# Optimization experiments

Measured on AMD Instinct MI355X. Metric: run time of the kernel, lower is better.

## Reference

```python
import jax, jax.numpy as jnp
import numpy as np

N, K, D, M, P, HG, HD = 120000, 8, 64, 100000, 16, 32, 96
VOXEL, TAU, OCC_INC, LMIN, LMAX = 0.1, 0.3, 0.5, -2.0, 3.5


def setup_inputs() -> dict:
    ks = jax.random.split(jax.random.key(0), 20)
    f32 = jnp.float32
    s = 0.05
    return {
        'pts_xyz': jax.random.uniform(ks[0], (N, 3), f32) * 10.0,
        'f_pts': jax.random.normal(ks[1], (N, D), f32),
        'z_latent': jax.random.normal(ks[2], (M, D), f32),
        'vals_st': jax.random.normal(ks[3], (M,), f32) * 0.5,
        'centers_xyz': jax.random.uniform(ks[4], (M, 3), f32) * 10.0,
        'Wf': jax.random.normal(ks[5], (P, D), f32) * s,
        'Wz': jax.random.normal(ks[6], (P, D), f32) * s,
        'w_delta': jax.random.normal(ks[7], (1, 3), f32) * s,
        'b_delta': jnp.zeros((1,), f32),
        'log_temp': jnp.zeros((1,), f32),
        'W_ih': jax.random.normal(ks[8], (3 * D, D), f32) * s,
        'W_hh': jax.random.normal(ks[9], (3 * D, D), f32) * s,
        'b_ih': jnp.zeros((3 * D,), f32),
        'b_hh': jnp.zeros((3 * D,), f32),
        'Wg1': jax.random.normal(ks[10], (HG, 2 * D), f32) * s,
        'bg1': jnp.zeros((HG,), f32),
        'Wg2': jax.random.normal(ks[11], (1, HG), f32) * s,
        'bg2': jnp.zeros((1,), f32),
        'ln_g': jnp.ones((D,), f32),
        'ln_b': jnp.zeros((D,), f32),
        'Wd1': jax.random.normal(ks[12], (HD, D), f32) * s,
        'bd1': jnp.zeros((HD,), f32),
        'Wd2': jax.random.normal(ks[13], (HD, HD), f32) * s,
        'bd2': jnp.zeros((HD,), f32),
        'Wd3': jax.random.normal(ks[14], (1, HD), f32) * s,
        'bd3': jnp.zeros((1,), f32),
        'keys': jnp.sort(jax.random.randint(ks[15], (M,), 0, 2 ** 30, jnp.int32)),
        'cand_idx': jax.random.randint(ks[16], (N, K), 0, M, jnp.int32),
    }


def _forward(pts_xyz, f_pts, z_latent, vals_st, centers_xyz, Wf, Wz, w_delta, b_delta,
             log_temp, W_ih, W_hh, b_ih, b_hh, Wg1, bg1, Wg2, bg2, ln_g, ln_b,
             Wd1, bd1, Wd2, bd2, Wd3, bd3, keys, cand_idx):
    # --- sparse voxel hash lookup + log-odds scatter update ---
    ijk = jnp.floor(pts_xyz / VOXEL).astype(jnp.int32)
    off = jnp.int32(1 << 9)
    h = ((ijk[:, 0] + off) << 20) ^ ((ijk[:, 1] + off) << 10) ^ (ijk[:, 2] + off)
    vox_idx = jnp.clip(jnp.searchsorted(keys, h), 0, M - 1)  # (N,)
    vals_new = jnp.clip(vals_st.at[vox_idx].add(OCC_INC), LMIN, LMAX)

    # --- top-K low-temperature routing: sim(f, z, delta) ---
    z_c = z_latent[cand_idx]                                  # (N,K,D) gather
    delta = pts_xyz[:, None, :] - centers_xyz[cand_idx]       # (N,K,3)
    Fp = f_pts @ Wf.T                                         # (N,P)
    Zp = z_c @ Wz.T                                           # (N,K,P)
    Fp = Fp / (jnp.linalg.norm(Fp, axis=-1, keepdims=True) + 1e-6)
    Zp = Zp / (jnp.linalg.norm(Zp, axis=-1, keepdims=True) + 1e-6)
    core = jnp.einsum('np,nkp->nk', Fp, Zp)
    dterm = jnp.einsum('nkc,c->nk', delta, w_delta[0]) + b_delta[0]
    sim = jnp.exp(log_temp[0]) * (core + dterm)
    w = jax.nn.softmax(sim / TAU, axis=-1)                    # (N,K)

    # --- scatter weighted point features to voxels ---
    flat_idx = cand_idx.reshape(-1)                           # (N*K,)
    contrib = (w[..., None] * f_pts[:, None, :]).reshape(-1, D)
    msg = jax.ops.segment_sum(contrib, flat_idx, num_segments=M)   # (M,D)
    wsum = jax.ops.segment_sum(w.reshape(-1), flat_idx, num_segments=M)
    msg = msg / (wsum[:, None] + 1e-6)

    # --- per-voxel gate + GRU latent fusion ---
    gate_in = jnp.concatenate([z_latent, msg], axis=-1)       # (M,2D)
    g = jax.nn.sigmoid(jax.nn.relu(gate_in @ Wg1.T + bg1) @ Wg2.T + bg2)  # (M,1)
    gi = msg @ W_ih.T + b_ih
    gh = z_latent @ W_hh.T + b_hh
    gir, giz, gin = jnp.split(gi, 3, axis=-1)
    ghr, ghz, ghn = jnp.split(gh, 3, axis=-1)
    r = jax.nn.sigmoid(gir + ghr)
    u = jax.nn.sigmoid(giz + ghz)
    n = jnp.tanh(gin + r * ghn)
    h_new = (1.0 - u) * n + u * z_latent
    z_new = z_latent + g * (h_new - z_latent)                 # (M,D)

    # --- decode occupancy: LN -> fc1 -> residual fc2 -> fc3 -> sigmoid ---
    mu = z_new.mean(-1, keepdims=True)
    var = z_new.var(-1, keepdims=True)
    x = (z_new - mu) * jax.lax.rsqrt(var + 1e-5) * ln_g + ln_b
    hd = jax.nn.relu(x @ Wd1.T + bd1)
    hd = hd + jax.nn.relu(hd @ Wd2.T + bd2)
    p = jax.nn.sigmoid((hd @ Wd3.T + bd3)[:, 0])              # (M,)

    return jnp.concatenate([p, vals_new])                     # (2M,)


def reference(pts_xyz, f_pts, z_latent, vals_st, centers_xyz, Wf, Wz, w_delta, b_delta,
              log_temp, W_ih, W_hh, b_ih, b_hh, Wg1, bg1, Wg2, bg2, ln_g, ln_b,
              Wd1, bd1, Wd2, bd2, Wd3, bd3, keys, cand_idx):
    return _forward(pts_xyz, f_pts, z_latent, vals_st, centers_xyz, Wf, Wz, w_delta,
                    b_delta, log_temp, W_ih, W_hh, b_ih, b_hh, Wg1, bg1, Wg2, bg2,
                    ln_g, ln_b, Wd1, bd1, Wd2, bd2, Wd3, bd3, keys, cand_idx)
```

## Files before the change

kernel.cpp:

```cpp
#include <hip/hip_runtime.h>
#include <math.h>

#define Nn 120000
#define Kk 8
#define Dd 64
#define Mm 100000
#define Pp 16
#define HGg 32
#define HDd 96
#define CAP 40
#define LUTB 12

typedef __attribute__((ext_vector_type(8))) short bf16x8;
typedef __attribute__((ext_vector_type(4))) float f32x4;
typedef __attribute__((ext_vector_type(4))) float fx4;
typedef __attribute__((ext_vector_type(4))) int ix4;

#define PB_K0    1563
#define PB_PREP  (PB_K0 + 3750)
#define PB_PACK  (PB_PREP + 22)
#define PB_INIT  (PB_PACK + 391)

__device__ __forceinline__ float sigmoidf_(float x) { return 1.f / (1.f + __expf(-x)); }
__device__ __forceinline__ float tanh_fast(float x) {
    float e = __expf(2.f * x);
    return 1.f - 2.f / (e + 1.f);
}
__device__ __forceinline__ short f2bf(float f) {
    unsigned u = __float_as_uint(f);
    unsigned r = (u + 0x7fffu + ((u >> 16) & 1u)) >> 16;
    return (short)r;
}

__global__ __launch_bounds__(256) void k_prep_all(const float* __restrict__ z,
                                                  const float* __restrict__ Wz,
                                                  const float* __restrict__ centers,
                                                  const float* __restrict__ w_delta,
                                                  const int* __restrict__ keys,
                                                  const float* __restrict__ f_pts,
                                                  const float* __restrict__ Wg1,
                                                  const float* __restrict__ W_ih,
                                                  const float* __restrict__ W_hh,
                                                  const float* __restrict__ Wd1,
                                                  const float* __restrict__ Wd2,
                                                  const float* __restrict__ vals,
                                                  unsigned* __restrict__ Zbf,
                                                  float* __restrict__ cdot,
                                                  int* __restrict__ lut,
                                                  signed char* __restrict__ f8,
                                                  short* __restrict__ wsW,
                                                  int* __restrict__ cnt,
                                                  float* __restrict__ vacc) {
    int b = blockIdx.x;
    if (b < PB_K0) {
        int g = threadIdx.x & 3;
        int m = b * 64 + (threadIdx.x >> 2);
        if (m >= Mm) return;
        if (g == 0 && m <= (1 << LUTB)) {
            int target = m << (30 - LUTB);
            int lo = 0, hi = Mm;
            while (lo < hi) {
                int mid = (lo + hi) >> 1;
                if (keys[mid] < target) lo = mid + 1; else hi = mid;
            }
            lut[m] = lo;
        }
        const float4* zr = (const float4*)(z + (size_t)m * Dd + g * 16);
        float4 q0 = zr[0], q1 = zr[1], q2 = zr[2], q3 = zr[3];
        float acc[Pp];
#pragma unroll
        for (int p = 0; p < Pp; p++) {
            const float4* w = (const float4*)(Wz + (size_t)p * Dd + g * 16);
            float4 w0 = w[0], w1 = w[1], w2 = w[2], w3 = w[3];
            float s = q0.x * w0.x + q0.y * w0.y + q0.z * w0.z + q0.w * w0.w;
            s += q1.x * w1.x + q1.y * w1.y + q1.z * w1.z + q1.w * w1.w;
            s += q2.x * w2.x + q2.y * w2.y + q2.z * w2.z + q2.w * w2.w;
            s += q3.x * w3.x + q3.y * w3.y + q3.z * w3.z + q3.w * w3.w;
            acc[p] = s;
        }
#pragma unroll
        for (int p = 0; p < Pp; p++) {
            acc[p] += __shfl_xor(acc[p], 1, 64);
            acc[p] += __shfl_xor(acc[p], 2, 64);
        }
        float ss = 0.f;
#pragma unroll
        for (int p = 0; p < Pp; p++) ss = fmaf(acc[p], acc[p], ss);
        float inv = 1.f / (sqrtf(ss) + 1e-6f);
        unsigned* row = Zbf + (size_t)m * 8;
        if (g < 2) {
            uint4 o;
            unsigned w[4];
#pragma unroll
            for (int j = 0; j < 4; j++) {
                float v0 = acc[g * 8 + 2 * j] * inv;
                float v1 = acc[g * 8 + 2 * j + 1] * inv;
                w[j] = (unsigned)(unsigned short)f2bf(v0)
                     | ((unsigned)(unsigned short)f2bf(v1) << 16);
            }
            o.x = w[0]; o.y = w[1]; o.z = w[2]; o.w = w[3];
            ((uint4*)row)[g] = o;
        } else if (g == 2) {
            cdot[m] = centers[3 * m] * w_delta[0] + centers[3 * m + 1] * w_delta[1]
                    + centers[3 * m + 2] * w_delta[2];
        }
    } else if (b < PB_PREP) {
        int i = (b - PB_K0) * 256 + threadIdx.x;
        int e = i * 8;
        const fx4* src = (const fx4*)(f_pts + e);
        fx4 a = __builtin_nontemporal_load(src);
        fx4 bb = __builtin_nontemporal_load(src + 1);
        float v[8] = {a.x, a.y, a.z, a.w, bb.x, bb.y, bb.z, bb.w};
        unsigned lo = 0, hi = 0;
#pragma unroll
        for (int j = 0; j < 4; j++) {
            int q = (int)rintf(fminf(fmaxf(v[j], -4.f), 4.f) * 32.f);
            lo |= ((unsigned)q & 0xffu) << (8 * j);
        }
#pragma unroll
        for (int j = 0; j < 4; j++) {
            int q = (int)rintf(fminf(fmaxf(v[4 + j], -4.f), 4.f) * 32.f);
            hi |= ((unsigned)q & 0xffu) << (8 * j);
        }
        *(int2*)(f8 + e) = make_int2((int)lo, (int)hi);
    } else if (b < PB_PACK) {
        int idx = (b - PB_PREP) * 256 + threadIdx.x;
        if (idx >= 86 * 64) return;
        int f = idx >> 6, lane = idx & 63;
        int lrow = lane & 15, lhi = lane >> 4;
        const float* src;
        int t, c, K;
        if (f < 8)       { int g = f;      t = g >> 2; c = g & 3;  src = Wg1;  K = 128; }
        else if (f < 32) { int g = f - 8;  t = g >> 1; c = g & 1;  src = W_ih; K = 64; }
        else if (f < 56) { int g = f - 32; t = g >> 1; c = g & 1;  src = W_hh; K = 64; }
        else if (f < 68) { int g = f - 56; t = g >> 1; c = g & 1;  src = Wd1;  K = 64; }
        else             { int g = f - 68; t = g / 3;  c = g % 3;  src = Wd2;  K = 96; }
        int o = t * 16 + lrow;
        int k0 = c * 32 + lhi * 8;
        short* dst = wsW + ((size_t)f * 64 + lane) * 8;
#pragma unroll
        for (int j = 0; j < 8; j++) dst[j] = f2bf(src[(size_t)o * K + k0 + j]);
    } else {
        int m = (b - PB_PACK) * 256 + threadIdx.x;
        if (m < Mm) {
            cnt[m] = 0;
            vacc[m] = vals[m];
        }
    }
}

__global__ __launch_bounds__(256) void k1_route(const float* __restrict__ pts,
                                                const float* __restrict__ f_pts,
                                                const float* __restrict__ Wf,
                                                const float* __restrict__ w_delta,
                                                const float* __restrict__ b_delta,
                                                const float* __restrict__ log_temp,
                                                const int* __restrict__ keys,
                                                const int* __restrict__ cand,
                                                const unsigned* __restrict__ Zbf,
                                                const float* __restrict__ cdot,
                                                const int* __restrict__ lut,
                                                float* __restrict__ vacc,
                                                int* __restrict__ cnt,
                                                int2* __restrict__ rec) {
    int g = threadIdx.x & 7;
    int n = blockIdx.x * 32 + (threadIdx.x >> 3);

    float px = pts[3 * n], py = pts[3 * n + 1], pz = pts[3 * n + 2];
    int myid = __builtin_nontemporal_load(cand + (size_t)n * Kk + g);

    if (g == 0) {
        int ix = (int)floorf(px / 0.1f);
        int iy = (int)floorf(py / 0.1f);
        int iz = (int)floorf(pz / 0.1f);
        int h = ((ix + 512) << 20) ^ ((iy + 512) << 10) ^ (iz + 512);
        int pfx = h >> (30 - LUTB);
        int lo = lut[pfx], hi = lut[pfx + 1];
        while (lo < hi) {
            int mid = (lo + hi) >> 1;
            if (keys[mid] < h) lo = mid + 1; else hi = mid;
        }
        int vi = lo < (Mm - 1) ? lo : (Mm - 1);
        atomicAdd(vacc + vi, 0.5f);
    }

    const fx4* fr = (const fx4*)(f_pts + (size_t)n * Dd + g * 8);
    fx4 q0 = __builtin_nontemporal_load(fr);
    fx4 q1 = __builtin_nontemporal_load(fr + 1);
    float fp[Pp];
#pragma unroll
    for (int p = 0; p < Pp; p++) {
        const float4* w = (const float4*)(Wf + (size_t)p * Dd + g * 8);
        float4 w0 = w[0], w1 = w[1];
        float s = q0.x * w0.x + q0.y * w0.y + q0.z * w0.z + q0.w * w0.w;
        s += q1.x * w1.x + q1.y * w1.y + q1.z * w1.z + q1.w * w1.w;
        fp[p] = s;
    }
#pragma unroll
    for (int p = 0; p < Pp; p++) {
        fp[p] += __shfl_xor(fp[p], 1, 64);
        fp[p] += __shfl_xor(fp[p], 2, 64);
        fp[p] += __shfl_xor(fp[p], 4, 64);
    }
    float ss = 0.f;
#pragma unroll
    for (int p = 0; p < Pp; p++) ss = fmaf(fp[p], fp[p], ss);
    float inv = 1.f / (sqrtf(ss) + 1e-6f);
#pragma unroll
    for (int p = 0; p < Pp; p++) fp[p] *= inv;

    float et = expf(log_temp[0]);
    float pdot = px * w_delta[0] + py * w_delta[1] + pz * w_delta[2] + b_delta[0];

    const uint4* zp = (const uint4*)(Zbf + (size_t)myid * 8);
    uint4 A = zp[0], B = zp[1];
    float cd = cdot[myid];
    unsigned uw[8] = {A.x, A.y, A.z, A.w, B.x, B.y, B.z, B.w};
    float core = 0.f;
#pragma unroll
    for (int j = 0; j < 8; j++) {
        float lo = __uint_as_float(uw[j] << 16);
        float hi = __uint_as_float(uw[j] & 0xffff0000u);
        core = fmaf(fp[2 * j], lo, core);
        core = fmaf(fp[2 * j + 1], hi, core);
    }
    float sim = et * (core + pdot - cd) / 0.3f;

    float mx = sim;
    mx = fmaxf(mx, __shfl_xor(mx, 1, 64));
    mx = fmaxf(mx, __shfl_xor(mx, 2, 64));
    mx = fmaxf(mx, __shfl_xor(mx, 4, 64));
    float e = __expf(sim - mx);
    float se = e;
    se += __shfl_xor(se, 1, 64);
    se += __shfl_xor(se, 2, 64);
    se += __shfl_xor(se, 4, 64);
    float w = e / se;

    int pos = atomicAdd(cnt + myid, 1);
    if (pos < CAP) {
        long long pk = (unsigned)n | ((long long)(unsigned)__float_as_int(w) << 32);
        __builtin_nontemporal_store(pk, (long long*)(rec + (size_t)myid * CAP + pos));
    }
}

__global__ __launch_bounds__(256) void k2_reduce(const signed char* __restrict__ f8,
                                                 const int* __restrict__ cnt,
                                                 const int2* __restrict__ rec,
                                                 unsigned short* __restrict__ msgb) {
    int wv = threadIdx.x >> 6, lane = threadIdx.x & 63;
    int m = blockIdx.x * 4 + wv;
    int c = cnt[m];
    if (c > CAP) c = CAP;
    const ix4* r4 = (const ix4*)(rec + (size_t)m * CAP);
    float acc = 0.f, wsum = 0.f;
    for (int i0 = 0; i0 < c; i0 += 8) {
        ix4 A = __builtin_nontemporal_load(r4 + (i0 >> 1) + 0);
        ix4 B = __builtin_nontemporal_load(r4 + (i0 >> 1) + 1);
        ix4 C = __builtin_nontemporal_load(r4 + (i0 >> 1) + 2);
        ix4 D = __builtin_nontemporal_load(r4 + (i0 >> 1) + 3);
        int nn[8];
        float ww[8];
        int rn[8] = {A.x, A.z, B.x, B.z, C.x, C.z, D.x, D.z};
        int rw[8] = {A.y, A.w, B.y, B.w, C.y, C.w, D.y, D.w};
#pragma unroll
        for (int k = 0; k < 8; k++) {
            bool valid = (i0 + k) < c;
            nn[k] = valid ? rn[k] : 0;
            ww[k] = valid ? __int_as_float(rw[k]) : 0.f;
        }
        float vv[8];
#pragma unroll
        for (int k = 0; k < 8; k++)
            vv[k] = (float)f8[((size_t)nn[k] << 6) + lane];
#pragma unroll
        for (int k = 0; k < 8; k++) {
            wsum += ww[k];
            acc = fmaf(ww[k], vv[k], acc);
        }
    }
    acc *= 0.03125f;
    msgb[(size_t)m * Dd + lane] = (unsigned short)f2bf(acc / (wsum + 1e-6f));
}

__global__ __launch_bounds__(256, 3) void k3_mfma(const float* __restrict__ z_latent,
                                                  const unsigned short* __restrict__ msgb,
                                                  const short* __restrict__ wsW,
                                                  const float* __restrict__ bg1,
                                                  const float* __restrict__ Wg2,
                                                  const float* __restrict__ bg2,
                                                  const float* __restrict__ b_ih,
                                                  const float* __restrict__ b_hh,
                                                  const float* __restrict__ ln_g,
                                                  const float* __restrict__ ln_b,
                                                  const float* __restrict__ bd1,
                                                  const float* __restrict__ bd2,
                                                  const float* __restrict__ Wd3,
                                                  const float* __restrict__ bd3,
                                                  const float* __restrict__ vacc,
                                                  float* __restrict__ out) {
    __shared__ float scr_all[4][16 * 97];
    int wv = threadIdx.x >> 6, lane = threadIdx.x & 63;
    int tile = blockIdx.x * 4 + wv;
    if (tile >= Mm / 16) return;
    int m0 = tile * 16;
    float* scr = scr_all[wv];
    int lrow = lane & 15;
    int lhi = lane >> 4;

    if (lane < 16) {
        float v = vacc[m0 + lane];
        out[Mm + m0 + lane] = fminf(fmaxf(v, -2.f), 3.5f);
    }

    const bf16x8* WF = (const bf16x8*)wsW;
#define BFRAG(off) (WF[(off) * 64 + lane])

    bf16x8 za[2], ma[2];
    const float* zrow = z_latent + (size_t)(m0 + lrow) * Dd + lhi * 8;
    const bf16x8* mrow = (const bf16x8*)(msgb + (size_t)(m0 + lrow) * Dd + lhi * 8);
#pragma unroll
    for (int c = 0; c < 2; c++) {
        bf16x8 t0;
#pragma unroll
        for (int j = 0; j < 8; j++) t0[j] = f2bf(zrow[c * 32 + j]);
        za[c] = t0;
        ma[c] = mrow[c * 4];
    }

    bf16x8 wgf[8];
#pragma unroll
    for (int j = 0; j < 8; j++) wgf[j] = BFRAG(j);
    f32x4 g0 = {0.f, 0.f, 0.f, 0.f}, g1 = {0.f, 0.f, 0.f, 0.f};
    bf16x8 gateA[4] = {za[0], za[1], ma[0], ma[1]};
#pragma unroll
    for (int c = 0; c < 4; c++) {
        g0 = __builtin_amdgcn_mfma_f32_16x16x32_bf16(gateA[c], wgf[c], g0, 0, 0, 0);
        g1 = __builtin_amdgcn_mfma_f32_16x16x32_bf16(gateA[c], wgf[4 + c], g1, 0, 0, 0);
    }
    float bgA = bg1[lrow], bgB = bg1[16 + lrow];
    float w2A = Wg2[lrow], w2B = Wg2[16 + lrow];
    float g[4];
#pragma unroll
    for (int r = 0; r < 4; r++) {
        float ga = fmaxf(g0[r] + bgA, 0.f) * w2A + fmaxf(g1[r] + bgB, 0.f) * w2B;
        ga += __shfl_xor(ga, 1, 64);
        ga += __shfl_xor(ga, 2, 64);
        ga += __shfl_xor(ga, 4, 64);
        ga += __shfl_xor(ga, 8, 64);
        g[r] = sigmoidf_(ga + bg2[0]);
    }

    float zn[4][4];
    float ps[4] = {0.f, 0.f, 0.f, 0.f}, pq[4] = {0.f, 0.f, 0.f, 0.f};
#pragma unroll
    for (int t = 0; t < 4; t++) {
        bf16x8 wt[12];
#pragma unroll
        for (int c = 0; c < 2; c++) {
            wt[0 + c]  = BFRAG(8 + t * 2 + c);
            wt[2 + c]  = BFRAG(8 + (t + 4) * 2 + c);
            wt[4 + c]  = BFRAG(8 + (t + 8) * 2 + c);
            wt[6 + c]  = BFRAG(32 + t * 2 + c);
            wt[8 + c]  = BFRAG(32 + (t + 4) * 2 + c);
            wt[10 + c] = BFRAG(32 + (t + 8) * 2 + c);
        }
        f32x4 Ar = {0.f, 0.f, 0.f, 0.f}, Az = Ar, An = Ar, Br = Ar, Bz = Ar, Bn = Ar;
#pragma unroll
        for (int c = 0; c < 2; c++) {
            Ar = __builtin_amdgcn_mfma_f32_16x16x32_bf16(ma[c], wt[0 + c], Ar, 0, 0, 0);
            Az = __builtin_amdgcn_mfma_f32_16x16x32_bf16(ma[c], wt[2 + c], Az, 0, 0, 0);
            An = __builtin_amdgcn_mfma_f32_16x16x32_bf16(ma[c], wt[4 + c], An, 0, 0, 0);
            Br = __builtin_amdgcn_mfma_f32_16x16x32_bf16(za[c], wt[6 + c], Br, 0, 0, 0);
            Bz = __builtin_amdgcn_mfma_f32_16x16x32_bf16(za[c], wt[8 + c], Bz, 0, 0, 0);
            Bn = __builtin_amdgcn_mfma_f32_16x16x32_bf16(za[c], wt[10 + c], Bn, 0, 0, 0);
        }
        int oc = t * 16 + lrow;
        float bir = b_ih[oc], biz = b_ih[64 + oc], bin = b_ih[128 + oc];
        float bhr = b_hh[oc], bhz = b_hh[64 + oc], bhn = b_hh[128 + oc];
#pragma unroll
        for (int r = 0; r < 4; r++) {
            int row = lhi * 4 + r;
            float zo = z_latent[(size_t)(m0 + row) * Dd + oc];
            float rr = sigmoidf_(Ar[r] + bir + Br[r] + bhr);
            float uu = sigmoidf_(Az[r] + biz + Bz[r] + bhz);
            float nnv = tanh_fast(An[r] + bin + rr * (Bn[r] + bhn));
            float hn = (1.f - uu) * nnv + uu * zo;
            float z2 = zo + g[r] * (hn - zo);
            zn[t][r] = z2;
            ps[r] += z2;
            pq[r] = fmaf(z2, z2, pq[r]);
        }
    }
    float mu[4], rs[4];
#pragma unroll
    for (int r = 0; r < 4; r++) {
        float s = ps[r], q = pq[r];
        s += __shfl_xor(s, 1, 64); q += __shfl_xor(q, 1, 64);
        s += __shfl_xor(s, 2, 64); q += __shfl_xor(q, 2, 64);
        s += __shfl_xor(s, 4, 64); q += __shfl_xor(q, 4, 64);
        s += __shfl_xor(s, 8, 64); q += __shfl_xor(q, 8, 64);
        float m = s * (1.f / 64.f);
        float v = q * (1.f / 64.f) - m * m;
        mu[r] = m;
        rs[r] = rsqrtf(v + 1e-5f);
    }
#pragma unroll
    for (int t = 0; t < 4; t++) {
        int o = t * 16 + lrow;
        float lg = ln_g[o], lb = ln_b[o];
#pragma unroll
        for (int r = 0; r < 4; r++)
            scr[(lhi * 4 + r) * 97 + o] = (zn[t][r] - mu[r]) * rs[r] * lg + lb;
    }
    __threadfence_block();

    bf16x8 xa[2];
#pragma unroll
    for (int c = 0; c < 2; c++) {
        bf16x8 tb;
#pragma unroll
        for (int j = 0; j < 8; j++) tb[j] = f2bf(scr[lrow * 97 + c * 32 + lhi * 8 + j]);
        xa[c] = tb;
    }
    bf16x8 wf1[12];
#pragma unroll
    for (int j = 0; j < 12; j++) wf1[j] = BFRAG(56 + j);
    f32x4 h1t[6];
#pragma unroll
    for (int t = 0; t < 6; t++) h1t[t] = (f32x4){0.f, 0.f, 0.f, 0.f};
#pragma unroll
    for (int t = 0; t < 6; t++)
#pragma unroll
        for (int c = 0; c < 2; c++)
            h1t[t] = __builtin_amdgcn_mfma_f32_16x16x32_bf16(xa[c], wf1[t * 2 + c], h1t[t], 0, 0, 0);
    float h1r[6][4];
#pragma unroll
    for (int t = 0; t < 6; t++) {
        float bb = bd1[t * 16 + lrow];
#pragma unroll
        for (int r = 0; r < 4; r++) {
            h1r[t][r] = fmaxf(h1t[t][r] + bb, 0.f);
            scr[(lhi * 4 + r) * 97 + t * 16 + lrow] = h1r[t][r];
        }
    }
    __threadfence_block();

    bf16x8 ha[3];
#pragma unroll
    for (int c = 0; c < 3; c++) {
        bf16x8 tb;
#pragma unroll
        for (int j = 0; j < 8; j++) tb[j] = f2bf(scr[lrow * 97 + c * 32 + lhi * 8 + j]);
        ha[c] = tb;
    }
    bf16x8 wf2[18];
#pragma unroll
    for (int j = 0; j < 18; j++) wf2[j] = BFRAG(68 + j);
    f32x4 o2[6];
#pragma unroll
    for (int t = 0; t < 6; t++) o2[t] = (f32x4){0.f, 0.f, 0.f, 0.f};
#pragma unroll
    for (int t = 0; t < 6; t++)
#pragma unroll
        for (int c = 0; c < 3; c++)
            o2[t] = __builtin_amdgcn_mfma_f32_16x16x32_bf16(ha[c], wf2[t * 3 + c], o2[t], 0, 0, 0);
    float pacc[4] = {0.f, 0.f, 0.f, 0.f};
#pragma unroll
    for (int t = 0; t < 6; t++) {
        int o = t * 16 + lrow;
        float bb = bd2[o], w3 = Wd3[o];
#pragma unroll
        for (int r = 0; r < 4; r++) {
            float hd2 = h1r[t][r] + fmaxf(o2[t][r] + bb, 0.f);
            pacc[r] = fmaf(hd2, w3, pacc[r]);
        }
    }
#pragma unroll
    for (int r = 0; r < 4; r++) {
        float s = pacc[r];
        s += __shfl_xor(s, 1, 64);
        s += __shfl_xor(s, 2, 64);
        s += __shfl_xor(s, 4, 64);
        s += __shfl_xor(s, 8, 64);
        if (lrow == 0) out[m0 + lhi * 4 + r] = sigmoidf_(s + bd3[0]);
    }
#undef BFRAG
}

extern "C" void kernel_launch(void* const* d_in, const int* in_sizes, int n_in,
                              void* d_out, int out_size, void* d_ws, size_t ws_size,
                              hipStream_t stream) {
    const float* pts      = (const float*)d_in[0];
    const float* f_pts    = (const float*)d_in[1];
    const float* z_lat    = (const float*)d_in[2];
    const float* vals     = (const float*)d_in[3];
    const float* centers  = (const float*)d_in[4];
    const float* Wf       = (const float*)d_in[5];
    const float* Wz       = (const float*)d_in[6];
    const float* w_delta  = (const float*)d_in[7];
    const float* b_delta  = (const float*)d_in[8];
    const float* log_temp = (const float*)d_in[9];
    const float* W_ih     = (const float*)d_in[10];
    const float* W_hh     = (const float*)d_in[11];
    const float* b_ih     = (const float*)d_in[12];
    const float* b_hh     = (const float*)d_in[13];
    const float* Wg1      = (const float*)d_in[14];
    const float* bg1      = (const float*)d_in[15];
    const float* Wg2      = (const float*)d_in[16];
    const float* bg2      = (const float*)d_in[17];
    const float* ln_g     = (const float*)d_in[18];
    const float* ln_b     = (const float*)d_in[19];
    const float* Wd1      = (const float*)d_in[20];
    const float* bd1      = (const float*)d_in[21];
    const float* Wd2      = (const float*)d_in[22];
    const float* bd2      = (const float*)d_in[23];
    const float* Wd3      = (const float*)d_in[24];
    const float* bd3      = (const float*)d_in[25];
    const int*   keys     = (const int*)d_in[26];
    const int*   cand     = (const int*)d_in[27];
    float* out = (float*)d_out;

    float* ws = (float*)d_ws;
    short* wsW = (short*)ws;
    unsigned* Zbf = (unsigned*)(ws + 32768);
    float* cdot = ws + 32768 + 800000;
    signed char* f8 = (signed char*)(ws + 32768 + 900000);
    float* base = ws + 32768 + 900000 + 1920000;
    unsigned short* msgb = (unsigned short*)base;
    float* vacc = base + (size_t)Mm * Dd / 2;
    int*   cnt  = (int*)(vacc + Mm);
    int2*  rec  = (int2*)(cnt + Mm);
    int*   lut  = (int*)((int*)rec + (size_t)Mm * CAP * 2);

    k_prep_all<<<PB_INIT, 256, 0, stream>>>(z_lat, Wz, centers, w_delta, keys, f_pts,
                                            Wg1, W_ih, W_hh, Wd1, Wd2, vals,
                                            Zbf, cdot, lut, f8, wsW, cnt, vacc);
    k1_route<<<Nn / 32, 256, 0, stream>>>(pts, f_pts, Wf, w_delta, b_delta, log_temp,
                                          keys, cand, Zbf, cdot, lut, vacc, cnt, rec);
    k2_reduce<<<Mm / 4, 256, 0, stream>>>(f8, cnt, rec, msgb);
    k3_mfma<<<(Mm / 16 + 3) / 4, 256, 0, stream>>>(z_lat, msgb, wsW, bg1, Wg2, bg2,
                                                   b_ih, b_hh, ln_g, ln_b, bd1, bd2,
                                                   Wd3, bd3, vacc, out);
}
```

Before: 311.1 us.

## Precompute normalized Wf projection in prep pass and enlarge hash LUT

The per-point Wf projection and L2 normalization now run once in the prep kernel's f_pts quantization blocks, which already read f_pts. The result is stored as a 16-float vector per point in a buffer aliased over the msgb region, so k1_route reads 64 bytes per point instead of the full 256-byte f_pts row and issues its gather loads earlier. The search-key lookup table grows from 12 to 16 bits and is built by its own dedicated blocks, which should shorten each binary search. The trade-off is extra writes and reads of the fpb buffer and more prep blocks, and the buffer reuse relies on msgb not being written until k2.

```diff
diff --git a/kernel.cpp b/kernel.cpp
--- a/kernel.cpp
+++ b/kernel.cpp
@@ -9,7 +9,7 @@
 #define HGg 32
 #define HDd 96
 #define CAP 40
-#define LUTB 12
+#define LUTB 16
 
 typedef __attribute__((ext_vector_type(8))) short bf16x8;
 typedef __attribute__((ext_vector_type(4))) float f32x4;
@@ -20,6 +20,7 @@
 #define PB_PREP  (PB_K0 + 3750)
 #define PB_PACK  (PB_PREP + 22)
 #define PB_INIT  (PB_PACK + 391)
+#define PB_LUT   (PB_INIT + 257)
 
 __device__ __forceinline__ float sigmoidf_(float x) { return 1.f / (1.f + __expf(-x)); }
 __device__ __forceinline__ float tanh_fast(float x) {
@@ -38,6 +39,7 @@
                                                   const float* __restrict__ w_delta,
                                                   const int* __restrict__ keys,
                                                   const float* __restrict__ f_pts,
+                                                  const float* __restrict__ Wf,
                                                   const float* __restrict__ Wg1,
                                                   const float* __restrict__ W_ih,
                                                   const float* __restrict__ W_hh,
@@ -48,6 +50,7 @@
                                                   float* __restrict__ cdot,
                                                   int* __restrict__ lut,
                                                   signed char* __restrict__ f8,
+                                                  float* __restrict__ fpb,
                                                   short* __restrict__ wsW,
                                                   int* __restrict__ cnt,
                                                   float* __restrict__ vacc) {
@@ -56,15 +59,6 @@
         int g = threadIdx.x & 3;
         int m = b * 64 + (threadIdx.x >> 2);
         if (m >= Mm) return;
-        if (g == 0 && m <= (1 << LUTB)) {
-            int target = m << (30 - LUTB);
-            int lo = 0, hi = Mm;
-            while (lo < hi) {
-                int mid = (lo + hi) >> 1;
-                if (keys[mid] < target) lo = mid + 1; else hi = mid;
-            }
-            lut[m] = lo;
-        }
         const float4* zr = (const float4*)(z + (size_t)m * Dd + g * 16);
         float4 q0 = zr[0], q1 = zr[1], q2 = zr[2], q3 = zr[3];
         float acc[Pp];
@@ -106,6 +100,7 @@
         }
     } else if (b < PB_PREP) {
         int i = (b - PB_K0) * 256 + threadIdx.x;
+        int g = i & 7;
         int e = i * 8;
         const fx4* src = (const fx4*)(f_pts + e);
         fx4 a = __builtin_nontemporal_load(src);
@@ -123,6 +118,36 @@
             hi |= ((unsigned)q & 0xffu) << (8 * j);
         }
         *(int2*)(f8 + e) = make_int2((int)lo, (int)hi);
+
+        float fp[Pp];
+#pragma unroll
+        for (int p = 0; p < Pp; p++) {
+            const float4* w = (const float4*)(Wf + (size_t)p * Dd + g * 8);
+            float4 w0 = w[0], w1 = w[1];
+            float s = v[0] * w0.x + v[1] * w0.y + v[2] * w0.z + v[3] * w0.w;
+            s += v[4] * w1.x + v[5] * w1.y + v[6] * w1.z + v[7] * w1.w;
+            fp[p] = s;
+        }
+#pragma unroll
+        for (int p = 0; p < Pp; p++) {
+            fp[p] += __shfl_xor(fp[p], 1, 64);
+            fp[p] += __shfl_xor(fp[p], 2, 64);
+            fp[p] += __shfl_xor(fp[p], 4, 64);
+        }
+        float ss = 0.f;
+#pragma unroll
+        for (int p = 0; p < Pp; p++) ss = fmaf(fp[p], fp[p], ss);
+        float inv = 1.f / (sqrtf(ss) + 1e-6f);
+#pragma unroll
+        for (int p = 0; p < Pp; p++) fp[p] *= inv;
+        if (g < 4) {
+            float4 o;
+            if (g == 0)      o = make_float4(fp[0], fp[1], fp[2], fp[3]);
+            else if (g == 1) o = make_float4(fp[4], fp[5], fp[6], fp[7]);
+            else if (g == 2) o = make_float4(fp[8], fp[9], fp[10], fp[11]);
+            else             o = make_float4(fp[12], fp[13], fp[14], fp[15]);
+            ((float4*)(fpb + (size_t)(i >> 3) * 16))[g] = o;
+        }
     } else if (b < PB_PACK) {
         int idx = (b - PB_PREP) * 256 + threadIdx.x;
         if (idx >= 86 * 64) return;
@@ -140,18 +165,28 @@
         short* dst = wsW + ((size_t)f * 64 + lane) * 8;
 #pragma unroll
         for (int j = 0; j < 8; j++) dst[j] = f2bf(src[(size_t)o * K + k0 + j]);
-    } else {
+    } else if (b < PB_INIT) {
         int m = (b - PB_PACK) * 256 + threadIdx.x;
         if (m < Mm) {
             cnt[m] = 0;
             vacc[m] = vals[m];
         }
+    } else {
+        int idx = (b - PB_INIT) * 256 + threadIdx.x;
+        if (idx <= (1 << LUTB)) {
+            int target = idx << (30 - LUTB);
+            int lo = 0, hi = Mm;
+            while (lo < hi) {
+                int mid = (lo + hi) >> 1;
+                if (keys[mid] < target) lo = mid + 1; else hi = mid;
+            }
+            lut[idx] = lo;
+        }
     }
 }
 
 __global__ __launch_bounds__(256) void k1_route(const float* __restrict__ pts,
-                                                const float* __restrict__ f_pts,
-                                                const float* __restrict__ Wf,
+                                                const float* __restrict__ fpb,
                                                 const float* __restrict__ w_delta,
                                                 const float* __restrict__ b_delta,
                                                 const float* __restrict__ log_temp,
@@ -166,8 +201,13 @@
     int g = threadIdx.x & 7;
     int n = blockIdx.x * 32 + (threadIdx.x >> 3);
 
+    int myid = __builtin_nontemporal_load(cand + (size_t)n * Kk + g);
+    const uint4* zp = (const uint4*)(Zbf + (size_t)myid * 8);
+    uint4 A = zp[0], B = zp[1];
+    float cd = cdot[myid];
+    const float4* fr = (const float4*)(fpb + (size_t)n * 16);
+    float4 F0 = fr[0], F1 = fr[1], F2 = fr[2], F3 = fr[3];
     float px = pts[3 * n], py = pts[3 * n + 1], pz = pts[3 * n + 2];
-    int myid = __builtin_nontemporal_load(cand + (size_t)n * Kk + g);
 
     if (g == 0) {
         int ix = (int)floorf(px / 0.1f);
@@ -184,37 +224,11 @@
         atomicAdd(vacc + vi, 0.5f);
     }
 
-    const fx4* fr = (const fx4*)(f_pts + (size_t)n * Dd + g * 8);
-    fx4 q0 = __builtin_nontemporal_load(fr);
-    fx4 q1 = __builtin_nontemporal_load(fr + 1);
-    float fp[Pp];
-#pragma unroll
-    for (int p = 0; p < Pp; p++) {
-        const float4* w = (const float4*)(Wf + (size_t)p * Dd + g * 8);
-        float4 w0 = w[0], w1 = w[1];
-        float s = q0.x * w0.x + q0.y * w0.y + q0.z * w0.z + q0.w * w0.w;
-        s += q1.x * w1.x + q1.y * w1.y + q1.z * w1.z + q1.w * w1.w;
-        fp[p] = s;
-    }
-#pragma unroll
-    for (int p = 0; p < Pp; p++) {
-        fp[p] += __shfl_xor(fp[p], 1, 64);
-        fp[p] += __shfl_xor(fp[p], 2, 64);
-        fp[p] += __shfl_xor(fp[p], 4, 64);
-    }
-    float ss = 0.f;
-#pragma unroll
-    for (int p = 0; p < Pp; p++) ss = fmaf(fp[p], fp[p], ss);
-    float inv = 1.f / (sqrtf(ss) + 1e-6f);
-#pragma unroll
-    for (int p = 0; p < Pp; p++) fp[p] *= inv;
-
     float et = expf(log_temp[0]);
     float pdot = px * w_delta[0] + py * w_delta[1] + pz * w_delta[2] + b_delta[0];
 
-    const uint4* zp = (const uint4*)(Zbf + (size_t)myid * 8);
-    uint4 A = zp[0], B = zp[1];
-    float cd = cdot[myid];
+    float fp[16] = {F0.x, F0.y, F0.z, F0.w, F1.x, F1.y, F1.z, F1.w,
+                    F2.x, F2.y, F2.z, F2.w, F3.x, F3.y, F3.z, F3.w};
     unsigned uw[8] = {A.x, A.y, A.z, A.w, B.x, B.y, B.z, B.w};
     float core = 0.f;
 #pragma unroll
@@ -528,15 +542,16 @@
     signed char* f8 = (signed char*)(ws + 32768 + 900000);
     float* base = ws + 32768 + 900000 + 1920000;
     unsigned short* msgb = (unsigned short*)base;
+    float* fpb = base;
     float* vacc = base + (size_t)Mm * Dd / 2;
     int*   cnt  = (int*)(vacc + Mm);
     int2*  rec  = (int2*)(cnt + Mm);
     int*   lut  = (int*)((int*)rec + (size_t)Mm * CAP * 2);
 
-    k_prep_all<<<PB_INIT, 256, 0, stream>>>(z_lat, Wz, centers, w_delta, keys, f_pts,
-                                            Wg1, W_ih, W_hh, Wd1, Wd2, vals,
-                                            Zbf, cdot, lut, f8, wsW, cnt, vacc);
-    k1_route<<<Nn / 32, 256, 0, stream>>>(pts, f_pts, Wf, w_delta, b_delta, log_temp,
+    k_prep_all<<<PB_LUT, 256, 0, stream>>>(z_lat, Wz, centers, w_delta, keys, f_pts,
+                                           Wf, Wg1, W_ih, W_hh, Wd1, Wd2, vals,
+                                           Zbf, cdot, lut, f8, fpb, wsW, cnt, vacc);
+    k1_route<<<Nn / 32, 256, 0, stream>>>(pts, fpb, w_delta, b_delta, log_temp,
                                           keys, cand, Zbf, cdot, lut, vacc, cnt, rec);
     k2_reduce<<<Mm / 4, 256, 0, stream>>>(f8, cnt, rec, msgb);
     k3_mfma<<<(Mm / 16 + 3) / 4, 256, 0, stream>>>(z_lat, msgb, wsW, bg1, Wg2, bg2,
```

Result: slower. 324.8 us (+4.4%).

## Fuse message reduction into the MFMA GRU/decoder kernel via per-wave shared scratch

Applied to the files above, without the earlier changes.

Removes the separate k2_reduce kernel. Each wave in k3_mfma now gathers and weight-reduces the int8 features for its 16 voxels, one voxel per iteration, and writes the bf16 messages into its shared-memory scratch before the gate MFMAs read them back. This drops a kernel launch and the global round trip of the bf16 message buffer. The cost is lower parallelism in the reduction: the latency-bound gathers now run serially inside a wave over 16 voxels, with occupancy set by the MFMA kernel's launch bounds.

```diff
diff --git a/kernel.cpp b/kernel.cpp
--- a/kernel.cpp
+++ b/kernel.cpp
@@ -244,47 +244,10 @@
     }
 }
 
-__global__ __launch_bounds__(256) void k2_reduce(const signed char* __restrict__ f8,
-                                                 const int* __restrict__ cnt,
-                                                 const int2* __restrict__ rec,
-                                                 unsigned short* __restrict__ msgb) {
-    int wv = threadIdx.x >> 6, lane = threadIdx.x & 63;
-    int m = blockIdx.x * 4 + wv;
-    int c = cnt[m];
-    if (c > CAP) c = CAP;
-    const ix4* r4 = (const ix4*)(rec + (size_t)m * CAP);
-    float acc = 0.f, wsum = 0.f;
-    for (int i0 = 0; i0 < c; i0 += 8) {
-        ix4 A = __builtin_nontemporal_load(r4 + (i0 >> 1) + 0);
-        ix4 B = __builtin_nontemporal_load(r4 + (i0 >> 1) + 1);
-        ix4 C = __builtin_nontemporal_load(r4 + (i0 >> 1) + 2);
-        ix4 D = __builtin_nontemporal_load(r4 + (i0 >> 1) + 3);
-        int nn[8];
-        float ww[8];
-        int rn[8] = {A.x, A.z, B.x, B.z, C.x, C.z, D.x, D.z};
-        int rw[8] = {A.y, A.w, B.y, B.w, C.y, C.w, D.y, D.w};
-#pragma unroll
-        for (int k = 0; k < 8; k++) {
-            bool valid = (i0 + k) < c;
-            nn[k] = valid ? rn[k] : 0;
-            ww[k] = valid ? __int_as_float(rw[k]) : 0.f;
-        }
-        float vv[8];
-#pragma unroll
-        for (int k = 0; k < 8; k++)
-            vv[k] = (float)f8[((size_t)nn[k] << 6) + lane];
-#pragma unroll
-        for (int k = 0; k < 8; k++) {
-            wsum += ww[k];
-            acc = fmaf(ww[k], vv[k], acc);
-        }
-    }
-    acc *= 0.03125f;
-    msgb[(size_t)m * Dd + lane] = (unsigned short)f2bf(acc / (wsum + 1e-6f));
-}
-
 __global__ __launch_bounds__(256, 3) void k3_mfma(const float* __restrict__ z_latent,
-                                                  const unsigned short* __restrict__ msgb,
+                                                  const signed char* __restrict__ f8,
+                                                  const int* __restrict__ cnt,
+                                                  const int2* __restrict__ rec,
                                                   const short* __restrict__ wsW,
                                                   const float* __restrict__ bg1,
                                                   const float* __restrict__ Wg2,
@@ -313,19 +276,59 @@
         out[Mm + m0 + lane] = fminf(fmaxf(v, -2.f), 3.5f);
     }
 
+#pragma unroll 2
+    for (int v = 0; v < 16; v++) {
+        int m = m0 + v;
+        int c = cnt[m];
+        if (c > CAP) c = CAP;
+        const ix4* r4 = (const ix4*)(rec + (size_t)m * CAP);
+        float acc = 0.f, wsum = 0.f;
+        for (int i0 = 0; i0 < c; i0 += 8) {
+            ix4 A = __builtin_nontemporal_load(r4 + (i0 >> 1) + 0);
+            ix4 B = __builtin_nontemporal_load(r4 + (i0 >> 1) + 1);
+            ix4 C = __builtin_nontemporal_load(r4 + (i0 >> 1) + 2);
+            ix4 D = __builtin_nontemporal_load(r4 + (i0 >> 1) + 3);
+            int rn[8] = {A.x, A.z, B.x, B.z, C.x, C.z, D.x, D.z};
+            int rw[8] = {A.y, A.w, B.y, B.w, C.y, C.w, D.y, D.w};
+            int nn[8];
+            float ww[8];
+#pragma unroll
+            for (int k = 0; k < 8; k++) {
+                bool valid = (i0 + k) < c;
+                nn[k] = valid ? rn[k] : 0;
+                ww[k] = valid ? __int_as_float(rw[k]) : 0.f;
+            }
+            float vv[8];
+#pragma unroll
+            for (int k = 0; k < 8; k++)
+                vv[k] = (float)f8[((size_t)nn[k] << 6) + lane];
+#pragma unroll
+            for (int k = 0; k < 8; k++) {
+                wsum += ww[k];
+                acc = fmaf(ww[k], vv[k], acc);
+            }
+        }
+        acc *= 0.03125f;
+        unsigned mb = ((unsigned)(unsigned short)f2bf(acc / (wsum + 1e-6f))) << 16;
+        scr[v * 97 + lane] = __uint_as_float(mb);
+    }
+    __threadfence_block();
+
     const bf16x8* WF = (const bf16x8*)wsW;
 #define BFRAG(off) (WF[(off) * 64 + lane])
 
     bf16x8 za[2], ma[2];
     const float* zrow = z_latent + (size_t)(m0 + lrow) * Dd + lhi * 8;
-    const bf16x8* mrow = (const bf16x8*)(msgb + (size_t)(m0 + lrow) * Dd + lhi * 8);
 #pragma unroll
     for (int c = 0; c < 2; c++) {
-        bf16x8 t0;
-#pragma unroll
-        for (int j = 0; j < 8; j++) t0[j] = f2bf(zrow[c * 32 + j]);
+        bf16x8 t0, t1;
+#pragma unroll
+        for (int j = 0; j < 8; j++) {
+            t0[j] = f2bf(zrow[c * 32 + j]);
+            t1[j] = f2bf(scr[lrow * 97 + c * 32 + lhi * 8 + j]);
+        }
         za[c] = t0;
-        ma[c] = mrow[c * 4];
+        ma[c] = t1;
     }
 
     bf16x8 wgf[8];
@@ -527,7 +530,6 @@
     float* cdot = ws + 32768 + 800000;
     signed char* f8 = (signed char*)(ws + 32768 + 900000);
     float* base = ws + 32768 + 900000 + 1920000;
-    unsigned short* msgb = (unsigned short*)base;
     float* vacc = base + (size_t)Mm * Dd / 2;
     int*   cnt  = (int*)(vacc + Mm);
     int2*  rec  = (int2*)(cnt + Mm);
@@ -538,8 +540,7 @@
                                             Zbf, cdot, lut, f8, wsW, cnt, vacc);
     k1_route<<<Nn / 32, 256, 0, stream>>>(pts, f_pts, Wf, w_delta, b_delta, log_temp,
                                           keys, cand, Zbf, cdot, lut, vacc, cnt, rec);
-    k2_reduce<<<Mm / 4, 256, 0, stream>>>(f8, cnt, rec, msgb);
-    k3_mfma<<<(Mm / 16 + 3) / 4, 256, 0, stream>>>(z_lat, msgb, wsW, bg1, Wg2, bg2,
-                                                   b_ih, b_hh, ln_g, ln_b, bd1, bd2,
-                                                   Wd3, bd3, vacc, out);
+    k3_mfma<<<(Mm / 16 + 3) / 4, 256, 0, stream>>>(z_lat, f8, cnt, rec, wsW, bg1, Wg2,
+                                                   bg2, b_ih, b_hh, ln_g, ln_b, bd1,
+                                                   bd2, Wd3, bd3, vacc, out);
 }
```

Measured after the change: 357.6 us. +15.0%, slower.

## Fuse message reduction into MFMA kernel and quantize features inside routing

Applied to the files above, without the earlier changes.

Moves the int8 quantization of point features out of the prep kernel and into the routing kernel, which already loads those rows, so f_pts is no longer read twice. Merges the separate reduce kernel into the MFMA GRU/decoder kernel: each block gathers and reduces messages for its 64 voxels into shared memory and feeds them directly to the MFMA stage. This drops one launch and the global msgb round trip. In exchange, each thread now gathers 16 int8 values per neighbor with wider loads, which raises register pressure, and the launch bounds change to allow 4 blocks per CU.

```diff
diff --git a/kernel.cpp b/kernel.cpp
--- a/kernel.cpp
+++ b/kernel.cpp
@@ -17,8 +17,7 @@
 typedef __attribute__((ext_vector_type(4))) int ix4;
 
 #define PB_K0    1563
-#define PB_PREP  (PB_K0 + 3750)
-#define PB_PACK  (PB_PREP + 22)
+#define PB_PACK  (PB_K0 + 22)
 #define PB_INIT  (PB_PACK + 391)
 
 __device__ __forceinline__ float sigmoidf_(float x) { return 1.f / (1.f + __expf(-x)); }
@@ -37,7 +36,6 @@
                                                   const float* __restrict__ centers,
                                                   const float* __restrict__ w_delta,
                                                   const int* __restrict__ keys,
-                                                  const float* __restrict__ f_pts,
                                                   const float* __restrict__ Wg1,
                                                   const float* __restrict__ W_ih,
                                                   const float* __restrict__ W_hh,
@@ -47,7 +45,6 @@
                                                   unsigned* __restrict__ Zbf,
                                                   float* __restrict__ cdot,
                                                   int* __restrict__ lut,
-                                                  signed char* __restrict__ f8,
                                                   short* __restrict__ wsW,
                                                   int* __restrict__ cnt,
                                                   float* __restrict__ vacc) {
@@ -104,27 +101,8 @@
             cdot[m] = centers[3 * m] * w_delta[0] + centers[3 * m + 1] * w_delta[1]
                     + centers[3 * m + 2] * w_delta[2];
         }
-    } else if (b < PB_PREP) {
-        int i = (b - PB_K0) * 256 + threadIdx.x;
-        int e = i * 8;
-        const fx4* src = (const fx4*)(f_pts + e);
-        fx4 a = __builtin_nontemporal_load(src);
-        fx4 bb = __builtin_nontemporal_load(src + 1);
-        float v[8] = {a.x, a.y, a.z, a.w, bb.x, bb.y, bb.z, bb.w};
-        unsigned lo = 0, hi = 0;
-#pragma unroll
-        for (int j = 0; j < 4; j++) {
-            int q = (int)rintf(fminf(fmaxf(v[j], -4.f), 4.f) * 32.f);
-            lo |= ((unsigned)q & 0xffu) << (8 * j);
-        }
-#pragma unroll
-        for (int j = 0; j < 4; j++) {
-            int q = (int)rintf(fminf(fmaxf(v[4 + j], -4.f), 4.f) * 32.f);
-            hi |= ((unsigned)q & 0xffu) << (8 * j);
-        }
-        *(int2*)(f8 + e) = make_int2((int)lo, (int)hi);
     } else if (b < PB_PACK) {
-        int idx = (b - PB_PREP) * 256 + threadIdx.x;
+        int idx = (b - PB_K0) * 256 + threadIdx.x;
         if (idx >= 86 * 64) return;
         int f = idx >> 6, lane = idx & 63;
         int lrow = lane & 15, lhi = lane >> 4;
@@ -162,7 +140,8 @@
                                                 const int* __restrict__ lut,
                                                 float* __restrict__ vacc,
                                                 int* __restrict__ cnt,
-                                                int2* __restrict__ rec) {
+                                                int2* __restrict__ rec,
+                                                signed char* __restrict__ f8) {
     int g = threadIdx.x & 7;
     int n = blockIdx.x * 32 + (threadIdx.x >> 3);
 
@@ -187,6 +166,23 @@
     const fx4* fr = (const fx4*)(f_pts + (size_t)n * Dd + g * 8);
     fx4 q0 = __builtin_nontemporal_load(fr);
     fx4 q1 = __builtin_nontemporal_load(fr + 1);
+
+    {
+        float v[8] = {q0.x, q0.y, q0.z, q0.w, q1.x, q1.y, q1.z, q1.w};
+        unsigned lo = 0, hi = 0;
+#pragma unroll
+        for (int j = 0; j < 4; j++) {
+            int q = (int)rintf(fminf(fmaxf(v[j], -4.f), 4.f) * 32.f);
+            lo |= ((unsigned)q & 0xffu) << (8 * j);
+        }
+#pragma unroll
+        for (int j = 0; j < 4; j++) {
+            int q = (int)rintf(fminf(fmaxf(v[4 + j], -4.f), 4.f) * 32.f);
+            hi |= ((unsigned)q & 0xffu) << (8 * j);
+        }
+        *(int2*)(f8 + (size_t)n * Dd + g * 8) = make_int2((int)lo, (int)hi);
+    }
+
     float fp[Pp];
 #pragma unroll
     for (int p = 0; p < Pp; p++) {
@@ -244,64 +240,85 @@
     }
 }
 
-__global__ __launch_bounds__(256) void k2_reduce(const signed char* __restrict__ f8,
-                                                 const int* __restrict__ cnt,
-                                                 const int2* __restrict__ rec,
-                                                 unsigned short* __restrict__ msgb) {
-    int wv = threadIdx.x >> 6, lane = threadIdx.x & 63;
-    int m = blockIdx.x * 4 + wv;
-    int c = cnt[m];
-    if (c > CAP) c = CAP;
-    const ix4* r4 = (const ix4*)(rec + (size_t)m * CAP);
-    float acc = 0.f, wsum = 0.f;
-    for (int i0 = 0; i0 < c; i0 += 8) {
-        ix4 A = __builtin_nontemporal_load(r4 + (i0 >> 1) + 0);
-        ix4 B = __builtin_nontemporal_load(r4 + (i0 >> 1) + 1);
-        ix4 C = __builtin_nontemporal_load(r4 + (i0 >> 1) + 2);
-        ix4 D = __builtin_nontemporal_load(r4 + (i0 >> 1) + 3);
-        int nn[8];
-        float ww[8];
-        int rn[8] = {A.x, A.z, B.x, B.z, C.x, C.z, D.x, D.z};
-        int rw[8] = {A.y, A.w, B.y, B.w, C.y, C.w, D.y, D.w};
-#pragma unroll
-        for (int k = 0; k < 8; k++) {
-            bool valid = (i0 + k) < c;
-            nn[k] = valid ? rn[k] : 0;
-            ww[k] = valid ? __int_as_float(rw[k]) : 0.f;
-        }
-        float vv[8];
-#pragma unroll
-        for (int k = 0; k < 8; k++)
-            vv[k] = (float)f8[((size_t)nn[k] << 6) + lane];
-#pragma unroll
-        for (int k = 0; k < 8; k++) {
-            wsum += ww[k];
-            acc = fmaf(ww[k], vv[k], acc);
-        }
-    }
-    acc *= 0.03125f;
-    msgb[(size_t)m * Dd + lane] = (unsigned short)f2bf(acc / (wsum + 1e-6f));
-}
-
-__global__ __launch_bounds__(256, 3) void k3_mfma(const float* __restrict__ z_latent,
-                                                  const unsigned short* __restrict__ msgb,
-                                                  const short* __restrict__ wsW,
-                                                  const float* __restrict__ bg1,
-                                                  const float* __restrict__ Wg2,
-                                                  const float* __restrict__ bg2,
-                                                  const float* __restrict__ b_ih,
-                                                  const float* __restrict__ b_hh,
-                                                  const float* __restrict__ ln_g,
-                                                  const float* __restrict__ ln_b,
-                                                  const float* __restrict__ bd1,
-                                                  const float* __restrict__ bd2,
-                                                  const float* __restrict__ Wd3,
-                                                  const float* __restrict__ bd3,
-                                                  const float* __restrict__ vacc,
-                                                  float* __restrict__ out) {
+__global__ __launch_bounds__(256, 4) void k23_mfma(const float* __restrict__ z_latent,
+                                                   const signed char* __restrict__ f8,
+                                                   const int* __restrict__ cnt,
+                                                   const int2* __restrict__ rec,
+                                                   const short* __restrict__ wsW,
+                                                   const float* __restrict__ bg1,
+                                                   const float* __restrict__ Wg2,
+                                                   const float* __restrict__ bg2,
+                                                   const float* __restrict__ b_ih,
+                                                   const float* __restrict__ b_hh,
+                                                   const float* __restrict__ ln_g,
+                                                   const float* __restrict__ ln_b,
+                                                   const float* __restrict__ bd1,
+                                                   const float* __restrict__ bd2,
+                                                   const float* __restrict__ Wd3,
+                                                   const float* __restrict__ bd3,
+                                                   const float* __restrict__ vacc,
+                                                   float* __restrict__ out) {
+    __shared__ unsigned short msgs[64][72];
     __shared__ float scr_all[4][16 * 97];
-    int wv = threadIdx.x >> 6, lane = threadIdx.x & 63;
-    int tile = blockIdx.x * 4 + wv;
+    int tid = threadIdx.x;
+    int wv = tid >> 6, lane = tid & 63;
+    int b = blockIdx.x;
+
+    {
+        int v = tid >> 2;
+        int dq = (tid & 3) << 4;
+        int m = b * 64 + v;
+        if (m < Mm) {
+            int c = cnt[m];
+            if (c > CAP) c = CAP;
+            const ix4* r4 = (const ix4*)(rec + (size_t)m * CAP);
+            const signed char* fq = f8 + dq;
+            float acc[16];
+#pragma unroll
+            for (int d = 0; d < 16; d++) acc[d] = 0.f;
+            float wsum = 0.f;
+            for (int i0 = 0; i0 < c; i0 += 8) {
+                ix4 A = r4[(i0 >> 1) + 0];
+                ix4 B = r4[(i0 >> 1) + 1];
+                ix4 C = r4[(i0 >> 1) + 2];
+                ix4 D = r4[(i0 >> 1) + 3];
+                int rn[8] = {A.x, A.z, B.x, B.z, C.x, C.z, D.x, D.z};
+                int rw[8] = {A.y, A.w, B.y, B.w, C.y, C.w, D.y, D.w};
+                int nn[8];
+                float ww[8];
+#pragma unroll
+                for (int k = 0; k < 8; k++) {
+                    bool valid = (i0 + k) < c;
+                    nn[k] = valid ? rn[k] : 0;
+                    ww[k] = valid ? __int_as_float(rw[k]) : 0.f;
+                }
+                int4 G[8];
+#pragma unroll
+                for (int k = 0; k < 8; k++)
+                    G[k] = *(const int4*)(fq + ((size_t)nn[k] << 6));
+#pragma unroll
+                for (int k = 0; k < 8; k++) {
+                    wsum += ww[k];
+                    int gg[4] = {G[k].x, G[k].y, G[k].z, G[k].w};
+#pragma unroll
+                    for (int q = 0; q < 4; q++)
+#pragma unroll
+                        for (int j = 0; j < 4; j++) {
+                            float vv = (float)((signed char)((gg[q] >> (8 * j)) & 0xff));
+                            acc[q * 4 + j] = fmaf(ww[k], vv, acc[q * 4 + j]);
+                        }
+                }
+            }
+#pragma unroll
+            for (int d = 0; d < 16; d++) {
+                float a = acc[d] * 0.03125f;
+                msgs[v][dq + d] = (unsigned short)f2bf(a / (wsum + 1e-6f));
+            }
+        }
+    }
+    __syncthreads();
+
+    int tile = b * 4 + wv;
     if (tile >= Mm / 16) return;
     int m0 = tile * 16;
     float* scr = scr_all[wv];
@@ -318,14 +335,14 @@
 
     bf16x8 za[2], ma[2];
     const float* zrow = z_latent + (size_t)(m0 + lrow) * Dd + lhi * 8;
-    const bf16x8* mrow = (const bf16x8*)(msgb + (size_t)(m0 + lrow) * Dd + lhi * 8);
+    const unsigned short* mr = &msgs[wv * 16 + lrow][lhi * 8];
 #pragma unroll
     for (int c = 0; c < 2; c++) {
         bf16x8 t0;
 #pragma unroll
         for (int j = 0; j < 8; j++) t0[j] = f2bf(zrow[c * 32 + j]);
         za[c] = t0;
-        ma[c] = mrow[c * 4];
+        ma[c] = *(const bf16x8*)(mr + c * 32);
     }
 
     bf16x8 wgf[8];
@@ -527,19 +544,18 @@
     float* cdot = ws + 32768 + 800000;
     signed char* f8 = (signed char*)(ws + 32768 + 900000);
     float* base = ws + 32768 + 900000 + 1920000;
-    unsigned short* msgb = (unsigned short*)base;
     float* vacc = base + (size_t)Mm * Dd / 2;
     int*   cnt  = (int*)(vacc + Mm);
     int2*  rec  = (int2*)(cnt + Mm);
     int*   lut  = (int*)((int*)rec + (size_t)Mm * CAP * 2);
 
-    k_prep_all<<<PB_INIT, 256, 0, stream>>>(z_lat, Wz, centers, w_delta, keys, f_pts,
+    k_prep_all<<<PB_INIT, 256, 0, stream>>>(z_lat, Wz, centers, w_delta, keys,
                                             Wg1, W_ih, W_hh, Wd1, Wd2, vals,
-                                            Zbf, cdot, lut, f8, wsW, cnt, vacc);
+                                            Zbf, cdot, lut, wsW, cnt, vacc);
     k1_route<<<Nn / 32, 256, 0, stream>>>(pts, f_pts, Wf, w_delta, b_delta, log_temp,
-                                          keys, cand, Zbf, cdot, lut, vacc, cnt, rec);
-    k2_reduce<<<Mm / 4, 256, 0, stream>>>(f8, cnt, rec, msgb);
-    k3_mfma<<<(Mm / 16 + 3) / 4, 256, 0, stream>>>(z_lat, msgb, wsW, bg1, Wg2, bg2,
-                                                   b_ih, b_hh, ln_g, ln_b, bd1, bd2,
-                                                   Wd3, bd3, vacc, out);
+                                          keys, cand, Zbf, cdot, lut, vacc, cnt, rec,
+                                          f8);
+    k23_mfma<<<(Mm / 16 + 3) / 4, 256, 0, stream>>>(z_lat, f8, cnt, rec, wsW, bg1,
+                                                    Wg2, bg2, b_ih, b_hh, ln_g, ln_b,
+                                                    bd1, bd2, Wd3, bd3, vacc, out);
 }
```

After: 279.0 us. 1.11x faster.
